# Optimization experiments

Measured on AMD Instinct MI355X. Metric: run time of the kernel, lower is better.

## Reference

```python
import jax, jax.numpy as jnp
import numpy as np

S, B, T = 128, 1024, 96
E, H, HH, ATT = 64, 200, 100, 200
ACT, FLD = 32, 8
V_SRC, N_PROD, V_PRIM, N_FLD = 20000, 101, 10000, 64
DEC_IN = ACT + ATT + FLD + H  # 440


def setup_inputs() -> dict:
    key = jax.random.key(0)
    ks = jax.random.split(key, 24)
    rn = lambda k, shp: jax.random.normal(k, shp, dtype=jnp.float32) * 0.05
    sentences = jax.random.randint(ks[0], (S, B), 0, V_SRC)
    is_prod = jax.random.randint(ks[1], (T, B), 0, 2).astype(jnp.int32)
    prod_ids = jax.random.randint(ks[2], (T, B), 0, N_PROD)
    prim_ids = jax.random.randint(ks[3], (T, B), 0, V_PRIM)
    field_ids = jax.random.randint(ks[4], (T, B), 0, N_FLD)
    pt = jax.random.randint(ks[5], (T, B), 0, T)
    parent_t = jnp.minimum(pt, jnp.maximum(jnp.arange(T)[:, None] - 1, 0))  # parent < t
    return {
        'sentences': sentences, 'is_prod': is_prod, 'prod_ids': prod_ids,
        'prim_ids': prim_ids, 'field_ids': field_ids, 'parent_t': parent_t,
        'src_emb': rn(ks[6], (V_SRC, E)),
        'actprod_emb': rn(ks[7], (N_PROD, ACT)),
        'prim_emb': rn(ks[8], (V_PRIM, ACT)),
        'field_emb': rn(ks[9], (N_FLD, FLD)),
        'Wih_f': rn(ks[10], (4 * HH, E)), 'Whh_f': rn(ks[11], (4 * HH, HH)), 'b_f': rn(ks[12], (4 * HH,)),
        'Wih_b': rn(ks[13], (4 * HH, E)), 'Whh_b': rn(ks[14], (4 * HH, HH)), 'b_b': rn(ks[15], (4 * HH,)),
        'Wih_d': rn(ks[16], (4 * H, DEC_IN)), 'Whh_d': rn(ks[17], (4 * H, H)), 'b_d': rn(ks[18], (4 * H,)),
        'W_attn': rn(ks[19], (H, H)),
        'W_av': rn(ks[20], (ATT, 2 * H)),
    }


def _lstm_cell(z, c):
    i, f, g, o = jnp.split(z, 4, axis=-1)  # torch gate order i,f,g,o
    c = jax.nn.sigmoid(f) * c + jax.nn.sigmoid(i) * jnp.tanh(g)
    h = jax.nn.sigmoid(o) * jnp.tanh(c)
    return h, c


def _lstm_dir(x_emb, Wih, Whh, b, reverse):
    # x_emb: [S,B,E]; precompute input projections once
    xw = jnp.einsum('sbe,he->sbh', x_emb, Wih) + b
    nb = x_emb.shape[1]
    hh = Whh.shape[1]
    init = (jnp.zeros((nb, hh), x_emb.dtype), jnp.zeros((nb, hh), x_emb.dtype))
    def step(carry, xw_t):
        h, c = carry
        h, c = _lstm_cell(xw_t + h @ Whh.T, c)
        return (h, c), h
    (hT, cT), hs = jax.lax.scan(step, init, xw, reverse=reverse)
    return hs, hT, cT


def _forward(sentences, is_prod, prod_ids, prim_ids, field_ids, parent_t,
             src_emb, actprod_emb, prim_emb, field_emb,
             Wih_f, Whh_f, b_f, Wih_b, Whh_b, b_b,
             Wih_d, Whh_d, b_d, W_attn, W_av):
    nb = sentences.shape[1]
    nt = is_prod.shape[0]
    emb = src_emb[sentences]                       # [S,B,E]
    hs_f, hTf, cTf = _lstm_dir(emb, Wih_f, Whh_f, b_f, False)
    hs_b, hTb, cTb = _lstm_dir(emb, Wih_b, Whh_b, b_b, True)
    enc = jnp.concatenate([hs_f, hs_b], -1).transpose(1, 0, 2)   # [B,S,H]
    enc_att = enc @ W_attn.T                                     # [B,S,H]
    # replicate torch h0.view(-1, H) on [2,B,HH]
    h = jnp.stack([hTf, hTb]).reshape(-1, H)
    c = jnp.stack([cTf, cTb]).reshape(-1, H)
    Hbuf = jnp.zeros((nt, nb, H), enc.dtype)
    s_att0 = jnp.zeros((nb, ATT), enc.dtype)
    barange = jnp.arange(nb)

    def dec_step(carry, xs):
        h, c, s_att, Hbuf = carry
        t, ip, pid, prid, fid, ptid = xs
        a_tm1 = jnp.where(ip[:, None] == 1, actprod_emb[pid], prim_emb[prid])  # [B,32]
        nft = field_emb[fid]                                                   # [B,8]
        parent = Hbuf[ptid, barange]                                           # [B,H] irregular gather
        inp = jnp.concatenate([a_tm1, s_att, nft, parent], axis=-1)           # [B,440]
        inp = jnp.where(t > 0, inp, jnp.zeros_like(inp))
        h, c = _lstm_cell(inp @ Wih_d.T + h @ Whh_d.T + b_d, c)
        aw = jax.nn.softmax(jnp.einsum('bsh,bh->bs', enc_att, h), axis=-1)
        ctx = jnp.einsum('bs,bsh->bh', aw, enc)
        s_att = jnp.tanh(jnp.concatenate([ctx, h], axis=1) @ W_av.T)
        Hbuf = Hbuf.at[t].set(h)
        return (h, c, s_att, Hbuf), s_att

    xs = (jnp.arange(nt), is_prod, prod_ids, prim_ids, field_ids, parent_t)
    _, att_vecs = jax.lax.scan(dec_step, (h, c, s_att0, Hbuf), xs)
    return att_vecs  # [T,B,ATT]


def reference(sentences, is_prod, prod_ids, prim_ids, field_ids, parent_t,
              src_emb, actprod_emb, prim_emb, field_emb,
              Wih_f, Whh_f, b_f, Wih_b, Whh_b, b_b,
              Wih_d, Whh_d, b_d, W_attn, W_av):
    return _forward(sentences, is_prod, prod_ids, prim_ids, field_ids, parent_t,
                    src_emb, actprod_emb, prim_emb, field_emb,
                    Wih_f, Whh_f, b_f, Wih_b, Whh_b, b_b,
                    Wih_d, Whh_d, b_d, W_attn, W_av)
```

## Files before the change

### kernel.cpp

```cpp
#include <hip/hip_runtime.h>

#define S_LEN 128
#define B_N   1024
#define T_LEN 96
#define E_DIM 64
#define HH    100
#define H_DIM 200
#define ACT_D 32
#define FLD_D 8
#define ATT_D 200
#define DEC_IN 440
#define KTOT  640
#define G4H   800
#define G4HH  400
#define ENC_LD 224
#define KH_PAD 224
#define KC_PAD 416
#define NCOL_PAD 208

typedef unsigned int  u32;
typedef unsigned short u16;
typedef _Float16 f16;
typedef _Float16 f16x8 __attribute__((ext_vector_type(8)));
typedef float    f32x4 __attribute__((ext_vector_type(4)));

#define MFMA16(a,b,c) __builtin_amdgcn_mfma_f32_16x16x32_f16((a),(b),(c),0,0,0)

static __device__ __forceinline__ float lo_bf(u32 u){ union{u32 i; float f;}v; v.i = u<<16; return v.f; }
static __device__ __forceinline__ float hi_bf(u32 u){ union{u32 i; float f;}v; v.i = u & 0xffff0000u; return v.f; }
static __device__ __forceinline__ float sigf(float x){
  x = fminf(30.f, fmaxf(-30.f, x));
  return 1.f/(1.f + __expf(-x));
}
static __device__ __forceinline__ float tanhf_(float x){
  x = fminf(15.f, fmaxf(-15.f, x));
  float e = __expf(-2.f*x);
  return (1.f - e)/(1.f + e);
}

static __device__ __forceinline__ u16 f2bf(float f){
  union{float f; u32 i;} v; v.f = f;
  u32 r = v.i + 0x7fffu + ((v.i >> 16) & 1u);
  return (u16)(r >> 16);
}
__global__ void k_prep(u16* __restrict__ dst, const float* __restrict__ src,
                       int K, int C, int sk, int sc)
{
  int idx = blockIdx.x*256 + threadIdx.x;
  if (idx >= K*C) return;
  int k = idx / C, c = idx - k*C;
  dst[(size_t)(k>>2)*(4*C) + 4*c + (k&3)] = f2bf(src[(size_t)k*sk + (size_t)c*sc]);
}

__global__ void k_pack16(f16* __restrict__ dst, const float* __restrict__ src,
                         int Kld, int koff, int C, int K, int sk, int sc)
{
  int idx = blockIdx.x*256 + threadIdx.x;
  if (idx >= C*K) return;
  int c = idx / K, k = idx - c*K;
  dst[(size_t)c*Kld + koff + k] = (f16)src[(size_t)k*sk + (size_t)c*sc];
}

__global__ void k_zf16(f16* __restrict__ dst, int n)
{
  int idx = blockIdx.x*256 + threadIdx.x;
  if (idx < n) dst[idx] = (f16)0.f;
}

__global__ __launch_bounds__(512) void k_encoder(
    const int* __restrict__ sentences, const float* __restrict__ src_emb,
    const float* __restrict__ b_f, const float* __restrict__ b_b,
    const uint2* __restrict__ wihF, const uint2* __restrict__ whhF,
    const uint2* __restrict__ wihB, const uint2* __restrict__ whhB,
    f16* __restrict__ enc,
    float* __restrict__ hTf, float* __restrict__ cTf,
    float* __restrict__ hTb, float* __restrict__ cTb)
{
  const int tid = threadIdx.x;
  const int dir = blockIdx.x >> 7;
  const int bg  = blockIdx.x & 127;
  const int b0  = bg * 8;

  __shared__ alignas(16) float xs[8][E_DIM];
  __shared__ alignas(16) float hs[8][HH];
  __shared__ alignas(16) float zs[8][G4HH];

  const uint2* wih = dir ? wihB : wihF;
  const uint2* whh = dir ? whhB : whhF;
  const float* bias = dir ? b_b : b_f;

  for (int idx = tid; idx < 8*HH; idx += 512) ((float*)hs)[idx] = 0.f;
  float c0r = 0.f, c1r = 0.f;

  const int col = tid;
  const bool act = (col < G4HH);
  const float bias0 = act ? bias[col] : 0.f;

  __syncthreads();

  for (int step = 0; step < S_LEN; ++step) {
    const int s = dir ? (S_LEN-1-step) : step;
    {
      int r = tid >> 6, e = tid & 63;
      int tok = sentences[s*B_N + (b0 + r)];
      xs[r][e] = src_emb[(size_t)tok*E_DIM + e];
    }
    __syncthreads();

    if (act) {
      float acc[8];
      #pragma unroll
      for (int r = 0; r < 8; ++r) acc[r] = bias0;
      #pragma unroll 2
      for (int k4 = 0; k4 < E_DIM/4; ++k4) {
        uint2 u = wih[k4*G4HH + col];
        float w0 = lo_bf(u.x), w1 = hi_bf(u.x), w2 = lo_bf(u.y), w3 = hi_bf(u.y);
        #pragma unroll
        for (int r = 0; r < 8; ++r) {
          float4 xv = *(const float4*)&xs[r][4*k4];
          acc[r] += xv.x*w0 + xv.y*w1 + xv.z*w2 + xv.w*w3;
        }
      }
      #pragma unroll 2
      for (int k4 = 0; k4 < HH/4; ++k4) {
        uint2 u = whh[k4*G4HH + col];
        float w0 = lo_bf(u.x), w1 = hi_bf(u.x), w2 = lo_bf(u.y), w3 = hi_bf(u.y);
        #pragma unroll
        for (int r = 0; r < 8; ++r) {
          float4 hv = *(const float4*)&hs[r][4*k4];
          acc[r] += hv.x*w0 + hv.y*w1 + hv.z*w2 + hv.w*w3;
        }
      }
      #pragma unroll
      for (int r = 0; r < 8; ++r) zs[r][col] = acc[r];
    }
    __syncthreads();

    {
      int r = tid / HH, j = tid - r*HH;
      float c = sigf(zs[r][HH+j])*c0r + sigf(zs[r][j])*tanhf_(zs[r][2*HH+j]);
      float h = sigf(zs[r][3*HH+j])*tanhf_(c);
      c0r = c;
      hs[r][j] = h;
      enc[((size_t)(b0+r)*S_LEN + s)*ENC_LD + dir*HH + j] = (f16)h;
      if (tid < 8*HH - 512) {
        int idx2 = tid + 512;
        int r2 = idx2 / HH, j2 = idx2 - r2*HH;
        float c2 = sigf(zs[r2][HH+j2])*c1r + sigf(zs[r2][j2])*tanhf_(zs[r2][2*HH+j2]);
        float h2 = sigf(zs[r2][3*HH+j2])*tanhf_(c2);
        c1r = c2;
        hs[r2][j2] = h2;
        enc[((size_t)(b0+r2)*S_LEN + s)*ENC_LD + dir*HH + j2] = (f16)h2;
      }
    }
    __syncthreads();
  }

  float* hT = dir ? hTb : hTf;
  float* cT = dir ? cTb : cTf;
  {
    int r = tid / HH, j = tid - r*HH;
    hT[(b0+r)*HH + j] = hs[r][j];
    cT[(b0+r)*HH + j] = c0r;
    if (tid < 8*HH - 512) {
      int idx2 = tid + 512; int r2 = idx2 / HH, j2 = idx2 - r2*HH;
      hT[(b0+r2)*HH + j2] = hs[r2][j2];
      cT[(b0+r2)*HH + j2] = c1r;
    }
  }
}

__global__ __launch_bounds__(512, 2) void k_decoder(
  const int* __restrict__ is_prod, const int* __restrict__ prod_ids,
  const int* __restrict__ prim_ids, const int* __restrict__ field_ids,
  const int* __restrict__ parent_t,
  const float* __restrict__ actprod_emb, const float* __restrict__ prim_emb,
  const float* __restrict__ field_emb, const float* __restrict__ b_d,
  const f16* __restrict__ wall,
  const f16* __restrict__ wattn,
  const f16* __restrict__ wav,
  const f16* __restrict__ enc,
  const float* __restrict__ hTf, const float* __restrict__ cTf,
  const float* __restrict__ hTb, const float* __restrict__ cTb,
  f16* __restrict__ Hbuf, float* __restrict__ out)
{
  const int tid  = threadIdx.x;
  const int lane = tid & 63;
  const int wid  = tid >> 6;
  const int b0   = blockIdx.x * 8;
  const int arow = lane & 15;
  const int aoff = (lane >> 4) * 8;

  __shared__ alignas(16) f16   xa[8][KTOT];
  __shared__ alignas(16) f16   hg[8][KH_PAD];
  __shared__ alignas(16) f16   gA[8][KH_PAD];
  __shared__ alignas(16) f16   cat[8][KC_PAD];
  __shared__ alignas(16) float zs[8][G4H];
  __shared__ alignas(16) float aw[8][S_LEN];
  __shared__ alignas(16) float ctxp[2][8][H_DIM];
  __shared__ float biasd[G4H];

  for (int idx = tid; idx < G4H; idx += 512) biasd[idx] = b_d[idx];
  for (int idx = tid; idx < 8*24; idx += 512) {
    int r = idx / 24; hg[r][200 + idx%24] = (f16)0.f;
  }
  for (int idx = tid; idx < 8*16; idx += 512) {
    int r = idx / 16; cat[r][400 + idx%16] = (f16)0.f;
  }
  for (int idx = tid; idx < 8*ATT_D; idx += 512) {
    int r = idx / ATT_D; xa[r][ACT_D + idx%ATT_D] = (f16)0.f;
  }
  for (int idx = tid; idx < 8*H_DIM; idx += 512) {
    int r = idx / H_DIM, j = idx - r*H_DIM; int b = b0 + r;
    float v;
    if (b < 512) v = (j < HH) ? hTf[(2*b)*HH + j] : hTf[(2*b+1)*HH + (j-HH)];
    else { int bb = b-512; v = (j < HH) ? hTb[(2*bb)*HH + j] : hTb[(2*bb+1)*HH + (j-HH)]; }
    f16 hv = (f16)v;
    xa[r][DEC_IN + j] = hv; hg[r][j] = hv; cat[r][H_DIM + j] = hv;
  }
  float cst[4];
  #pragma unroll
  for (int kk = 0; kk < 4; ++kk) {
    int slot = tid + 512*kk;
    float v = 0.f;
    if (slot < 8*H_DIM) {
      int r = slot / H_DIM, j = slot - r*H_DIM; int b = b0 + r;
      if (b < 512) v = (j < HH) ? cTf[(2*b)*HH + j] : cTf[(2*b+1)*HH + (j-HH)];
      else { int bb = b-512; v = (j < HH) ? cTb[(2*bb)*HH + j] : cTb[(2*bb+1)*HH + (j-HH)]; }
    }
    cst[kk] = v;
  }
  __syncthreads();

  for (int t = 0; t < T_LEN; ++t) {
    for (int idx = tid; idx < 8*DEC_IN; idx += 512) {
      int r = idx / DEC_IN, k = idx - r*DEC_IN;
      if (k >= ACT_D && k < ACT_D + ATT_D) continue;
      f16 v = (f16)0.f;
      if (t > 0) {
        int b = b0 + r;
        if (k < ACT_D) {
          float f = (is_prod[t*B_N + b] == 1)
            ? actprod_emb[prod_ids[t*B_N + b]*ACT_D + k]
            : prim_emb[prim_ids[t*B_N + b]*ACT_D + k];
          v = (f16)f;
        } else if (k < ACT_D + ATT_D + FLD_D) {
          v = (f16)field_emb[field_ids[t*B_N + b]*FLD_D + (k - ACT_D - ATT_D)];
        } else {
          int pt = parent_t[t*B_N + b];
          v = Hbuf[((size_t)pt*B_N + b)*H_DIM + (k - (ACT_D+ATT_D+FLD_D))];
        }
      }
      xa[r][k] = v;
    }
    __syncthreads();

    {
      f16x8 afr[20];
      #pragma unroll
      for (int kk = 0; kk < 20; ++kk) {
        f16x8 v = {0,0,0,0,0,0,0,0};
        if (arow < 8) v = *(const f16x8*)&xa[arow][kk*32 + aoff];
        afr[kk] = v;
      }
      int t_begin = wid*6 + (wid < 2 ? wid : 2);
      int t_count = 6 + (wid < 2 ? 1 : 0);
      for (int ti = 0; ti < t_count; ti += 2) {
        int ta = t_begin + ti;
        bool hasb = (ti + 1 < t_count);
        int tb = hasb ? ta + 1 : ta;
        int ca = ta*16 + (lane & 15);
        int cb = tb*16 + (lane & 15);
        float bva = biasd[ca], bvb = biasd[cb];
        f32x4 acca = {bva, bva, bva, bva};
        f32x4 accb = {bvb, bvb, bvb, bvb};
        const f16* pa = wall + (size_t)ca*KTOT + aoff;
        const f16* pb = wall + (size_t)cb*KTOT + aoff;
        #pragma unroll
        for (int kk = 0; kk < 20; ++kk) {
          f16x8 Ba = *(const f16x8*)(pa + kk*32);
          f16x8 Bb = *(const f16x8*)(pb + kk*32);
          acca = MFMA16(afr[kk], Ba, acca);
          accb = MFMA16(afr[kk], Bb, accb);
        }
        if (lane < 32) {
          int rb = (lane >> 4) * 4;
          #pragma unroll
          for (int i2 = 0; i2 < 4; ++i2) zs[rb+i2][ca] = acca[i2];
          if (hasb) {
            #pragma unroll
            for (int i2 = 0; i2 < 4; ++i2) zs[rb+i2][cb] = accb[i2];
          }
        }
      }
    }
    __syncthreads();

    #pragma unroll
    for (int kk = 0; kk < 4; ++kk) {
      int slot = tid + 512*kk;
      if (slot < 8*H_DIM) {
        int r = slot / H_DIM, j = slot - r*H_DIM;
        float c = sigf(zs[r][H_DIM+j])*cst[kk] + sigf(zs[r][j])*tanhf_(zs[r][2*H_DIM+j]);
        float h = sigf(zs[r][3*H_DIM+j])*tanhf_(c);
        cst[kk] = c;
        f16 hv = (f16)h;
        xa[r][DEC_IN + j] = hv; hg[r][j] = hv; cat[r][H_DIM + j] = hv;
        Hbuf[((size_t)t*B_N + (b0+r))*H_DIM + j] = hv;
      }
    }
    __syncthreads();

    {
      f16x8 ga[7];
      #pragma unroll
      for (int kk = 0; kk < 7; ++kk) {
        f16x8 v = {0,0,0,0,0,0,0,0};
        if (arow < 8) v = *(const f16x8*)&hg[arow][kk*32 + aoff];
        ga[kk] = v;
      }
      #pragma unroll
      for (int pass = 0; pass < 2; ++pass) {
        int tt = wid + pass*8;
        if (tt < 13) {
          int c = tt*16 + (lane & 15);
          f32x4 acc = {0.f,0.f,0.f,0.f};
          const f16* p = wattn + (size_t)c*KH_PAD + aoff;
          #pragma unroll
          for (int kk = 0; kk < 7; ++kk)
            acc = MFMA16(ga[kk], *(const f16x8*)(p + kk*32), acc);
          if (lane < 32) {
            int rb = (lane >> 4) * 4;
            #pragma unroll
            for (int i2 = 0; i2 < 4; ++i2)
              if (c < H_DIM) gA[rb+i2][c] = (f16)acc[i2];
          }
        }
      }
    }
    __syncthreads();

    {
      int r = wid;
      const f16* gp = &gA[r][0];
      const f16* ep0 = enc + ((size_t)(b0+r)*S_LEN + lane)*ENC_LD;
      const f16* ep1 = ep0 + (size_t)64*ENC_LD;
      float s0v = 0.f, s1v = 0.f;
      #pragma unroll 5
      for (int o = 0; o < 25; ++o) {
        f16x8 g8 = *(const f16x8*)(gp + 8*o);
        f16x8 e0 = *(const f16x8*)(ep0 + 8*o);
        f16x8 e1 = *(const f16x8*)(ep1 + 8*o);
        #pragma unroll
        for (int i = 0; i < 8; ++i) {
          s0v += (float)e0[i] * (float)g8[i];
          s1v += (float)e1[i] * (float)g8[i];
        }
      }
      float m = fmaxf(s0v, s1v);
      #pragma unroll
      for (int d = 32; d; d >>= 1) m = fmaxf(m, __shfl_xor(m, d));
      float e0v = __expf(s0v - m), e1v = __expf(s1v - m);
      float sm = e0v + e1v;
      #pragma unroll
      for (int d = 32; d; d >>= 1) sm += __shfl_xor(sm, d);
      float rd = 1.f / sm;
      aw[r][lane]      = e0v * rd;
      aw[r][lane + 64] = e1v * rd;
    }
    __syncthreads();

    if (tid < 400) {
      int q = tid & 1, o = (tid >> 1) % 25, r = tid / 50;
      const f16* ep = enc + ((size_t)(b0+r)*S_LEN + q*64)*ENC_LD + 8*o;
      float acc[8] = {0.f,0.f,0.f,0.f,0.f,0.f,0.f,0.f};
      #pragma unroll 4
      for (int s2 = 0; s2 < 64; ++s2) {
        float w = aw[r][q*64 + s2];
        f16x8 e8 = *(const f16x8*)(ep + (size_t)s2*ENC_LD);
        #pragma unroll
        for (int i = 0; i < 8; ++i) acc[i] += w * (float)e8[i];
      }
      #pragma unroll
      for (int i = 0; i < 8; ++i) ctxp[q][r][8*o + i] = acc[i];
    }
    __syncthreads();

    #pragma unroll
    for (int kk = 0; kk < 4; ++kk) {
      int slot = tid + 512*kk;
      if (slot < 8*H_DIM) {
        int r = slot / H_DIM, cc = slot - r*H_DIM;
        cat[r][cc] = (f16)(ctxp[0][r][cc] + ctxp[1][r][cc]);
      }
    }
    __syncthreads();

    {
      f16x8 sa[13];
      #pragma unroll
      for (int kk = 0; kk < 13; ++kk) {
        f16x8 v = {0,0,0,0,0,0,0,0};
        if (arow < 8) v = *(const f16x8*)&cat[arow][kk*32 + aoff];
        sa[kk] = v;
      }
      #pragma unroll
      for (int pass = 0; pass < 2; ++pass) {
        int tt = wid + pass*8;
        if (tt < 13) {
          int c = tt*16 + (lane & 15);
          f32x4 acc = {0.f,0.f,0.f,0.f};
          const f16* p = wav + (size_t)c*KC_PAD + aoff;
          #pragma unroll
          for (int kk = 0; kk < 13; ++kk)
            acc = MFMA16(sa[kk], *(const f16x8*)(p + kk*32), acc);
          if (lane < 32 && c < ATT_D) {
            int rb = (lane >> 4) * 4;
            #pragma unroll
            for (int i2 = 0; i2 < 4; ++i2) {
              float v = tanhf_(acc[i2]);
              out[((size_t)t*B_N + (b0+rb+i2))*ATT_D + c] = v;
              xa[rb+i2][ACT_D + c] = (f16)v;
            }
          }
        }
      }
    }
    __syncthreads();
  }
}

extern "C" void kernel_launch(void* const* d_in, const int* in_sizes, int n_in,
                              void* d_out, int out_size, void* d_ws, size_t ws_size,
                              hipStream_t stream)
{
  const int*   sentences = (const int*)  d_in[0];
  const int*   is_prod   = (const int*)  d_in[1];
  const int*   prod_ids  = (const int*)  d_in[2];
  const int*   prim_ids  = (const int*)  d_in[3];
  const int*   field_ids = (const int*)  d_in[4];
  const int*   parent_t  = (const int*)  d_in[5];
  const float* src_emb   = (const float*)d_in[6];
  const float* actprod   = (const float*)d_in[7];
  const float* prim_emb  = (const float*)d_in[8];
  const float* field_emb = (const float*)d_in[9];
  const float* Wih_f = (const float*)d_in[10];
  const float* Whh_f = (const float*)d_in[11];
  const float* b_f   = (const float*)d_in[12];
  const float* Wih_b = (const float*)d_in[13];
  const float* Whh_b = (const float*)d_in[14];
  const float* b_b   = (const float*)d_in[15];
  const float* Wih_d = (const float*)d_in[16];
  const float* Whh_d = (const float*)d_in[17];
  const float* b_d   = (const float*)d_in[18];
  const float* W_attn= (const float*)d_in[19];
  const float* W_av  = (const float*)d_in[20];
  (void)in_sizes; (void)n_in; (void)out_size; (void)ws_size;

  char* ws = (char*)d_ws;
  size_t off = 0;
  auto take = [&](size_t bytes) -> void* {
    void* p = ws + off;
    off = (off + bytes + 255) & ~(size_t)255;
    return p;
  };
  u16* wihF = (u16*)take((size_t)64*400*2);
  u16* whhF = (u16*)take((size_t)100*400*2);
  u16* wihB = (u16*)take((size_t)64*400*2);
  u16* whhB = (u16*)take((size_t)100*400*2);
  f16* wall16  = (f16*)take((size_t)800*640*2);
  f16* wattn16 = (f16*)take((size_t)NCOL_PAD*KH_PAD*2);
  f16* wav16   = (f16*)take((size_t)NCOL_PAD*KC_PAD*2);
  f16* enc16   = (f16*)take((size_t)B_N*S_LEN*ENC_LD*2);
  float* hTf = (float*)take((size_t)B_N*HH*4);
  float* cTf = (float*)take((size_t)B_N*HH*4);
  float* hTb = (float*)take((size_t)B_N*HH*4);
  float* cTb = (float*)take((size_t)B_N*HH*4);
  f16* Hbuf16 = (f16*)take((size_t)T_LEN*B_N*H_DIM*2);
  float* outp = (float*)d_out;

  auto prep = [&](u16* dst, const float* src, int K, int C, int sk, int sc){
    int n = K*C;
    k_prep<<<(n+255)/256, 256, 0, stream>>>(dst, src, K, C, sk, sc);
  };
  prep(wihF, Wih_f, 64, 400, 1, 64);
  prep(whhF, Whh_f, 100, 400, 1, 100);
  prep(wihB, Wih_b, 64, 400, 1, 64);
  prep(whhB, Whh_b, 100, 400, 1, 100);

  {
    int n;
    n = NCOL_PAD*KH_PAD; k_zf16<<<(n+255)/256,256,0,stream>>>(wattn16, n);
    n = NCOL_PAD*KC_PAD; k_zf16<<<(n+255)/256,256,0,stream>>>(wav16, n);
    n = 800*440; k_pack16<<<(n+255)/256,256,0,stream>>>(wall16, Wih_d, KTOT, 0,   800, 440, 1, 440);
    n = 800*200; k_pack16<<<(n+255)/256,256,0,stream>>>(wall16, Whh_d, KTOT, 440, 800, 200, 1, 200);
    n = 200*200; k_pack16<<<(n+255)/256,256,0,stream>>>(wattn16, W_attn, KH_PAD, 0, 200, 200, 200, 1);
    n = 200*400; k_pack16<<<(n+255)/256,256,0,stream>>>(wav16, W_av, KC_PAD, 0, 200, 400, 1, 400);
  }

  hipMemsetAsync(enc16, 0, (size_t)B_N*S_LEN*ENC_LD*2, stream);

  k_encoder<<<256, 512, 0, stream>>>(sentences, src_emb, b_f, b_b,
      (const uint2*)wihF, (const uint2*)whhF, (const uint2*)wihB, (const uint2*)whhB,
      enc16, hTf, cTf, hTb, cTb);

  k_decoder<<<128, 512, 0, stream>>>(is_prod, prod_ids, prim_ids, field_ids, parent_t,
      actprod, prim_emb, field_emb, b_d,
      wall16, wattn16, wav16,
      enc16, hTf, cTf, hTb, cTb, Hbuf16, outp);
}
```

Before: 8.001 ms.

## Transpose encoder outputs to k-major layout and use MFMA for attention context

Adds a per-batch transpose kernel that stores encoder states as [b][k][s], so the decoder's attention-score pass has each lane group read contiguous sequence positions over a split of the hidden dimension. The softmax reduction moves to cross-lane shuffles, and the context vector is now computed with MFMA on f16 attention weights instead of scalar FMAs with a two-partial reduction through shared memory. Shared-memory row strides are padded to reduce bank conflicts. In exchange there is an extra transpose kernel and workspace buffer, attention weights are rounded to f16, and the context MFMA wastes most of its A rows because each step uses only one of 16 rows.

```diff
diff --git a/kernel.cpp b/kernel.cpp
--- a/kernel.cpp
+++ b/kernel.cpp
@@ -13,15 +13,20 @@
 #define KTOT  640
 #define G4H   800
 #define G4HH  400
-#define ENC_LD 224
 #define KH_PAD 224
 #define KC_PAD 416
 #define NCOL_PAD 208
+#define EK_ROWS 208
+#define XA_LD 648
+#define HG_LD 232
+#define GA_LD 232
+#define CAT_LD 424
 
 typedef unsigned int  u32;
 typedef unsigned short u16;
 typedef _Float16 f16;
 typedef _Float16 f16x8 __attribute__((ext_vector_type(8)));
+typedef _Float16 f16x4 __attribute__((ext_vector_type(4)));
 typedef float    f32x4 __attribute__((ext_vector_type(4)));
 
 #define MFMA16(a,b,c) __builtin_amdgcn_mfma_f32_16x16x32_f16((a),(b),(c),0,0,0)
@@ -67,12 +72,35 @@
   if (idx < n) dst[idx] = (f16)0.f;
 }
 
+__global__ __launch_bounds__(256) void k_transpose(
+    const f16* __restrict__ enc_sk, f16* __restrict__ enc_ks)
+{
+  __shared__ f16 ld[H_DIM][136];
+  const int b = blockIdx.x, tid = threadIdx.x;
+  const f16* src = enc_sk + (size_t)b*S_LEN*H_DIM;
+  for (int idx = tid; idx < S_LEN*(H_DIM/4); idx += 256) {
+    int s = idx / (H_DIM/4), jc = idx - s*(H_DIM/4);
+    f16x4 v = *(const f16x4*)(src + (size_t)s*H_DIM + 4*jc);
+    #pragma unroll
+    for (int i = 0; i < 4; ++i) ld[4*jc + i][s] = v[i];
+  }
+  __syncthreads();
+  f16* dst = enc_ks + (size_t)b*EK_ROWS*S_LEN;
+  for (int idx = tid; idx < H_DIM*(S_LEN/8); idx += 256) {
+    int k = idx / (S_LEN/8), so = idx - k*(S_LEN/8);
+    f16x8 v;
+    #pragma unroll
+    for (int i = 0; i < 8; ++i) v[i] = ld[k][8*so + i];
+    *(f16x8*)(dst + (size_t)k*S_LEN + 8*so) = v;
+  }
+}
+
 __global__ __launch_bounds__(512) void k_encoder(
     const int* __restrict__ sentences, const float* __restrict__ src_emb,
     const float* __restrict__ b_f, const float* __restrict__ b_b,
     const uint2* __restrict__ wihF, const uint2* __restrict__ whhF,
     const uint2* __restrict__ wihB, const uint2* __restrict__ whhB,
-    f16* __restrict__ enc,
+    f16* __restrict__ enc_sk,
     float* __restrict__ hTf, float* __restrict__ cTf,
     float* __restrict__ hTb, float* __restrict__ cTb)
 {
@@ -142,7 +170,7 @@
       float h = sigf(zs[r][3*HH+j])*tanhf_(c);
       c0r = c;
       hs[r][j] = h;
-      enc[((size_t)(b0+r)*S_LEN + s)*ENC_LD + dir*HH + j] = (f16)h;
+      enc_sk[((size_t)(b0+r)*S_LEN + s)*H_DIM + dir*HH + j] = (f16)h;
       if (tid < 8*HH - 512) {
         int idx2 = tid + 512;
         int r2 = idx2 / HH, j2 = idx2 - r2*HH;
@@ -150,7 +178,7 @@
         float h2 = sigf(zs[r2][3*HH+j2])*tanhf_(c2);
         c1r = c2;
         hs[r2][j2] = h2;
-        enc[((size_t)(b0+r2)*S_LEN + s)*ENC_LD + dir*HH + j2] = (f16)h2;
+        enc_sk[((size_t)(b0+r2)*S_LEN + s)*H_DIM + dir*HH + j2] = (f16)h2;
       }
     }
     __syncthreads();
@@ -179,7 +207,7 @@
   const f16* __restrict__ wall,
   const f16* __restrict__ wattn,
   const f16* __restrict__ wav,
-  const f16* __restrict__ enc,
+  const f16* __restrict__ enc_ks,
   const float* __restrict__ hTf, const float* __restrict__ cTf,
   const float* __restrict__ hTb, const float* __restrict__ cTb,
   f16* __restrict__ Hbuf, float* __restrict__ out)
@@ -191,24 +219,26 @@
   const int arow = lane & 15;
   const int aoff = (lane >> 4) * 8;
 
-  __shared__ alignas(16) f16   xa[8][KTOT];
-  __shared__ alignas(16) f16   hg[8][KH_PAD];
-  __shared__ alignas(16) f16   gA[8][KH_PAD];
-  __shared__ alignas(16) f16   cat[8][KC_PAD];
+  __shared__ alignas(16) f16   xa[8][XA_LD];
+  __shared__ alignas(16) f16   hg[8][HG_LD];
+  __shared__ alignas(16) f16   gA[8][GA_LD];
+  __shared__ alignas(16) f16   cat[8][CAT_LD];
+  __shared__ alignas(16) f16   aw_sh[8][S_LEN];
   __shared__ alignas(16) float zs[8][G4H];
-  __shared__ alignas(16) float aw[8][S_LEN];
-  __shared__ alignas(16) float ctxp[2][8][H_DIM];
   __shared__ float biasd[G4H];
 
   for (int idx = tid; idx < G4H; idx += 512) biasd[idx] = b_d[idx];
-  for (int idx = tid; idx < 8*24; idx += 512) {
-    int r = idx / 24; hg[r][200 + idx%24] = (f16)0.f;
-  }
-  for (int idx = tid; idx < 8*16; idx += 512) {
-    int r = idx / 16; cat[r][400 + idx%16] = (f16)0.f;
+  for (int idx = tid; idx < 8*(HG_LD-H_DIM); idx += 512) {
+    int n = HG_LD-H_DIM; hg[idx/n][H_DIM + idx%n] = (f16)0.f;
+  }
+  for (int idx = tid; idx < 8*(GA_LD-H_DIM); idx += 512) {
+    int n = GA_LD-H_DIM; gA[idx/n][H_DIM + idx%n] = (f16)0.f;
+  }
+  for (int idx = tid; idx < 8*(CAT_LD-2*H_DIM); idx += 512) {
+    int n = CAT_LD-2*H_DIM; cat[idx/n][2*H_DIM + idx%n] = (f16)0.f;
   }
   for (int idx = tid; idx < 8*ATT_D; idx += 512) {
-    int r = idx / ATT_D; xa[r][ACT_D + idx%ATT_D] = (f16)0.f;
+    xa[idx/ATT_D][ACT_D + idx%ATT_D] = (f16)0.f;
   }
   for (int idx = tid; idx < 8*H_DIM; idx += 512) {
     int r = idx / H_DIM, j = idx - r*H_DIM; int b = b0 + r;
@@ -269,8 +299,8 @@
         int ta = t_begin + ti;
         bool hasb = (ti + 1 < t_count);
         int tb = hasb ? ta + 1 : ta;
-        int ca = ta*16 + (lane & 15);
-        int cb = tb*16 + (lane & 15);
+        int ca = ta*16 + arow;
+        int cb = tb*16 + arow;
         float bva = biasd[ca], bvb = biasd[cb];
         f32x4 acca = {bva, bva, bva, bva};
         f32x4 accb = {bvb, bvb, bvb, bvb};
@@ -323,7 +353,7 @@
       for (int pass = 0; pass < 2; ++pass) {
         int tt = wid + pass*8;
         if (tt < 13) {
-          int c = tt*16 + (lane & 15);
+          int c = tt*16 + arow;
           f32x4 acc = {0.f,0.f,0.f,0.f};
           const f16* p = wattn + (size_t)c*KH_PAD + aoff;
           #pragma unroll
@@ -341,57 +371,66 @@
     __syncthreads();
 
     {
-      int r = wid;
-      const f16* gp = &gA[r][0];
-      const f16* ep0 = enc + ((size_t)(b0+r)*S_LEN + lane)*ENC_LD;
-      const f16* ep1 = ep0 + (size_t)64*ENC_LD;
-      float s0v = 0.f, s1v = 0.f;
-      #pragma unroll 5
-      for (int o = 0; o < 25; ++o) {
-        f16x8 g8 = *(const f16x8*)(gp + 8*o);
-        f16x8 e0 = *(const f16x8*)(ep0 + 8*o);
-        f16x8 e1 = *(const f16x8*)(ep1 + 8*o);
-        #pragma unroll
-        for (int i = 0; i < 8; ++i) {
-          s0v += (float)e0[i] * (float)g8[i];
-          s1v += (float)e1[i] * (float)g8[i];
-        }
-      }
-      float m = fmaxf(s0v, s1v);
-      #pragma unroll
-      for (int d = 32; d; d >>= 1) m = fmaxf(m, __shfl_xor(m, d));
-      float e0v = __expf(s0v - m), e1v = __expf(s1v - m);
-      float sm = e0v + e1v;
-      #pragma unroll
-      for (int d = 32; d; d >>= 1) sm += __shfl_xor(sm, d);
-      float rd = 1.f / sm;
-      aw[r][lane]      = e0v * rd;
-      aw[r][lane + 64] = e1v * rd;
-    }
-    __syncthreads();
-
-    if (tid < 400) {
-      int q = tid & 1, o = (tid >> 1) % 25, r = tid / 50;
-      const f16* ep = enc + ((size_t)(b0+r)*S_LEN + q*64)*ENC_LD + 8*o;
+      const int r = wid;
+      const int sl = lane & 15, kp = lane >> 4;
+      const f16* ep = enc_ks + ((size_t)(b0+r)*EK_ROWS + kp*52)*S_LEN + 8*sl;
+      const f16* gp = &gA[r][kp*52];
       float acc[8] = {0.f,0.f,0.f,0.f,0.f,0.f,0.f,0.f};
       #pragma unroll 4
-      for (int s2 = 0; s2 < 64; ++s2) {
-        float w = aw[r][q*64 + s2];
-        f16x8 e8 = *(const f16x8*)(ep + (size_t)s2*ENC_LD);
+      for (int i = 0; i < 52; ++i) {
+        f16x8 e8 = *(const f16x8*)(ep + (size_t)i*S_LEN);
+        float gf = (float)gp[i];
         #pragma unroll
-        for (int i = 0; i < 8; ++i) acc[i] += w * (float)e8[i];
-      }
-      #pragma unroll
-      for (int i = 0; i < 8; ++i) ctxp[q][r][8*o + i] = acc[i];
-    }
-    __syncthreads();
-
-    #pragma unroll
-    for (int kk = 0; kk < 4; ++kk) {
-      int slot = tid + 512*kk;
-      if (slot < 8*H_DIM) {
-        int r = slot / H_DIM, cc = slot - r*H_DIM;
-        cat[r][cc] = (f16)(ctxp[0][r][cc] + ctxp[1][r][cc]);
+        for (int q = 0; q < 8; ++q) acc[q] += gf * (float)e8[q];
+      }
+      #pragma unroll
+      for (int q = 0; q < 8; ++q) {
+        acc[q] += __shfl_xor(acc[q], 16);
+        acc[q] += __shfl_xor(acc[q], 32);
+      }
+      float m = acc[0];
+      #pragma unroll
+      for (int q = 1; q < 8; ++q) m = fmaxf(m, acc[q]);
+      #pragma unroll
+      for (int d = 1; d < 16; d <<= 1) m = fmaxf(m, __shfl_xor(m, d));
+      float e[8], sm = 0.f;
+      #pragma unroll
+      for (int q = 0; q < 8; ++q) { e[q] = __expf(acc[q] - m); sm += e[q]; }
+      #pragma unroll
+      for (int d = 1; d < 16; d <<= 1) sm += __shfl_xor(sm, d);
+      float rd = 1.f / sm;
+      if (kp == 0) {
+        f16x8 w;
+        #pragma unroll
+        for (int q = 0; q < 8; ++q) w[q] = (f16)(e[q] * rd);
+        *(f16x8*)&aw_sh[r][8*sl] = w;
+      }
+    }
+    __syncthreads();
+
+    {
+      #pragma unroll
+      for (int pass = 0; pass < 2; ++pass) {
+        int tt = wid + pass*8;
+        if (tt < 13) {
+          int c = tt*16 + arow;
+          f32x4 acc = {0.f,0.f,0.f,0.f};
+          const f16* eb = enc_ks + (size_t)b0*EK_ROWS*S_LEN + (size_t)c*S_LEN + aoff;
+          #pragma unroll 4
+          for (int kt = 0; kt < 32; ++kt) {
+            int rp = kt >> 2;
+            int s0 = (kt & 3) * 32;
+            f16x8 a = {0,0,0,0,0,0,0,0};
+            if (arow == rp) a = *(const f16x8*)&aw_sh[rp][s0 + aoff];
+            f16x8 bf = *(const f16x8*)(eb + (size_t)rp*EK_ROWS*S_LEN + s0);
+            acc = MFMA16(a, bf, acc);
+          }
+          if (lane < 32 && c < H_DIM) {
+            int rb = (lane >> 4) * 4;
+            #pragma unroll
+            for (int i2 = 0; i2 < 4; ++i2) cat[rb+i2][c] = (f16)acc[i2];
+          }
+        }
       }
     }
     __syncthreads();
@@ -408,7 +447,7 @@
       for (int pass = 0; pass < 2; ++pass) {
         int tt = wid + pass*8;
         if (tt < 13) {
-          int c = tt*16 + (lane & 15);
+          int c = tt*16 + arow;
           f32x4 acc = {0.f,0.f,0.f,0.f};
           const f16* p = wav + (size_t)c*KC_PAD + aoff;
           #pragma unroll
@@ -471,7 +510,8 @@
   f16* wall16  = (f16*)take((size_t)800*640*2);
   f16* wattn16 = (f16*)take((size_t)NCOL_PAD*KH_PAD*2);
   f16* wav16   = (f16*)take((size_t)NCOL_PAD*KC_PAD*2);
-  f16* enc16   = (f16*)take((size_t)B_N*S_LEN*ENC_LD*2);
+  f16* enc_sk  = (f16*)take((size_t)B_N*S_LEN*H_DIM*2);
+  f16* enc_ks  = (f16*)take((size_t)B_N*EK_ROWS*S_LEN*2);
   float* hTf = (float*)take((size_t)B_N*HH*4);
   float* cTf = (float*)take((size_t)B_N*HH*4);
   float* hTb = (float*)take((size_t)B_N*HH*4);
@@ -498,14 +538,14 @@
     n = 200*400; k_pack16<<<(n+255)/256,256,0,stream>>>(wav16, W_av, KC_PAD, 0, 200, 400, 1, 400);
   }
 
-  hipMemsetAsync(enc16, 0, (size_t)B_N*S_LEN*ENC_LD*2, stream);
-
   k_encoder<<<256, 512, 0, stream>>>(sentences, src_emb, b_f, b_b,
       (const uint2*)wihF, (const uint2*)whhF, (const uint2*)wihB, (const uint2*)whhB,
-      enc16, hTf, cTf, hTb, cTb);
+      enc_sk, hTf, cTf, hTb, cTb);
+
+  k_transpose<<<B_N, 256, 0, stream>>>(enc_sk, enc_ks);
 
   k_decoder<<<128, 512, 0, stream>>>(is_prod, prod_ids, prim_ids, field_ids, parent_t,
       actprod, prim_emb, field_emb, b_d,
       wall16, wattn16, wav16,
-      enc16, hTf, cTf, hTb, cTb, Hbuf16, outp);
-}
+      enc_ks, hTf, cTf, hTb, cTb, Hbuf16, outp);
+}
```

Measured after the change: 7.847 ms. About the same (-1.9%).
